# Optimization experiments

Hardware: AMD Instinct MI355X
Metric: run time of the kernel (lower is better)

The kernel has to match this reference:

```python
import jax, jax.numpy as jnp
import numpy as np

NEG_SLOPE = 0.2  # PyG GATConv default negative_slope
N_GRAPHS = 128


def gat_conv(x, src, dst, w, a_src, a_dst, b):
    """PyG GATConv (v1), concat=True. x:[N,F], src/dst:[E] (self-loops included),
    w:[F,H*C], a_src/a_dst:[H,C], b:[H*C]."""
    N = x.shape[0]
    H, C = a_src.shape
    h = (x @ w).reshape(N, H, C)                      # [N,H,C]
    e = (h * a_src).sum(-1)[src] + (h * a_dst).sum(-1)[dst]  # [E,H]
    e = jnp.where(e > 0, e, NEG_SLOPE * e)            # leaky_relu
    m = jax.ops.segment_max(e, dst, num_segments=N)   # per-dst softmax max
    ex = jnp.exp(e - m[dst])
    s = jax.ops.segment_sum(ex, dst, num_segments=N)
    alpha = ex / (s[dst] + 1e-16)                     # [E,H]
    out = jax.ops.segment_sum(h[src] * alpha[:, :, None], dst, num_segments=N)
    return out.reshape(N, H * C) + b


def pool(x, batch, num_graphs):
    """concat(global_mean_pool, global_max_pool)."""
    ones = jnp.ones((x.shape[0],), x.dtype)
    cnt = jax.ops.segment_sum(ones, batch, num_segments=num_graphs)
    mean = jax.ops.segment_sum(x, batch, num_segments=num_graphs) / jnp.maximum(cnt, 1.0)[:, None]
    mx = jax.ops.segment_max(x, batch, num_segments=num_graphs)
    return jnp.concatenate([mean, mx], axis=-1)


def setup_inputs() -> dict:
    key = jax.random.key(0)
    ks = jax.random.split(key, 30)
    N, E, G = 100000, 800000, N_GRAPHS
    F_in, H, C = 260, 4, 64
    HC = H * C  # 256

    def lin(k, i, o):
        return (jax.random.normal(k, (i, o), jnp.float32) * (1.0 / np.sqrt(i)))

    def att(k):
        return jax.random.normal(k, (H, C), jnp.float32) * 0.1

    return {
        "x": jax.random.normal(ks[0], (N, F_in), jnp.float32),
        "edge_index": jax.random.randint(ks[1], (2, E), 0, N),
        "batch": jnp.sort(jax.random.randint(ks[2], (N,), 0, G)),
        "gat1_w": lin(ks[3], F_in, HC), "gat1_as": att(ks[4]), "gat1_ad": att(ks[5]),
        "gat1_b": jnp.zeros((HC,), jnp.float32),
        "lin1_w": lin(ks[6], HC, C), "lin1_b": jnp.zeros((C,), jnp.float32),
        "gat2_w": lin(ks[7], C, HC), "gat2_as": att(ks[8]), "gat2_ad": att(ks[9]),
        "gat2_b": jnp.zeros((HC,), jnp.float32),
        "lin2_w": lin(ks[10], HC, C), "lin2_b": jnp.zeros((C,), jnp.float32),
        "sum_w": lin(ks[11], 4 * C, 2 * C), "sum_b": jnp.zeros((2 * C,), jnp.float32),
        "sh1_w": lin(ks[12], 2 * C, C), "sh1_b": jnp.zeros((C,), jnp.float32),
        "sh2_w": lin(ks[13], C, C), "sh2_b": jnp.zeros((C,), jnp.float32),
        "sh3_w": lin(ks[14], C, C), "sh3_b": jnp.zeros((C,), jnp.float32),
        "reg_w": lin(ks[15], C, 32), "reg_b": jnp.zeros((32,), jnp.float32),
    }


def reference(x, edge_index, batch,
              gat1_w, gat1_as, gat1_ad, gat1_b, lin1_w, lin1_b,
              gat2_w, gat2_as, gat2_ad, gat2_b, lin2_w, lin2_b,
              sum_w, sum_b, sh1_w, sh1_b, sh2_w, sh2_b, sh3_w, sh3_b,
              reg_w, reg_b):
    N = x.shape[0]
    loop = jnp.arange(N)
    src = jnp.concatenate([edge_index[0], loop])  # add_self_loops=True
    dst = jnp.concatenate([edge_index[1], loop])

    h = gat_conv(x, src, dst, gat1_w, gat1_as, gat1_ad, gat1_b)
    h = jax.nn.selu(h @ lin1_w + lin1_b)
    x1 = pool(h, batch, N_GRAPHS)                 # [G, 2C]

    h = gat_conv(h, src, dst, gat2_w, gat2_as, gat2_ad, gat2_b)
    h = jax.nn.selu(h @ lin2_w + lin2_b)
    x2 = pool(h, batch, N_GRAPHS)                 # [G, 2C]

    z = jnp.concatenate([x1, x2], axis=-1) @ sum_w + sum_b
    z = jax.nn.selu(z @ sh1_w + sh1_b)
    z = jax.nn.selu(z @ sh2_w + sh2_b)
    z = jax.nn.selu(z @ sh3_w + sh3_b)
    return z @ reg_w + reg_b                      # [G, 32]
```

## Files before the change

### kernel.cpp

```cpp
#include <hip/hip_runtime.h>
#include <hip/hip_bf16.h>
#include <cstdint>

#define NEG_SLOPE 0.2f
#define HEADS 4
#define CH 64
#define HC 256
#define F_IN 260
#define KPAD1 288
#define NGRAPH 128

typedef __attribute__((ext_vector_type(8))) short bf16x8;
typedef __attribute__((ext_vector_type(8))) unsigned short u16x8;
typedef __attribute__((ext_vector_type(4))) float f32x4;

__device__ __forceinline__ float seluf(float x){
    const float sc=1.0507009873554805f, al=1.6732632423543772f;
    return x>0.f ? sc*x : sc*al*(__expf(x)-1.f);
}
__device__ __forceinline__ unsigned fenc(float x){
    unsigned u=__float_as_uint(x);
    return (u&0x80000000u)? ~u : (u|0x80000000u);
}
__device__ __forceinline__ float fdec(unsigned e){
    unsigned u = (e&0x80000000u)? (e&0x7fffffffu) : ~e;
    return __uint_as_float(u);
}
__device__ __forceinline__ float bf2f(unsigned short u){
    return __uint_as_float(((unsigned)u)<<16);
}
__device__ __forceinline__ unsigned short f2bf_raw(float x){
    unsigned u = __float_as_uint(x);
    unsigned rounded = u + 0x7fffu + ((u >> 16) & 1u);
    return (unsigned short)(rounded >> 16);
}
__device__ __forceinline__ void gload_lds16(const void* g, void* l){
    __builtin_amdgcn_global_load_lds(
        (const __attribute__((address_space(1))) void*)g,
        (__attribute__((address_space(3))) void*)l, 16, 0, 0);
}

__global__ void fill_u32_kernel(unsigned* p, unsigned v, int n){
    int i = blockIdx.x*blockDim.x + threadIdx.x;
    for (; i<n; i += gridDim.x*blockDim.x) p[i]=v;
}

__global__ void degree_kernel(const int* __restrict__ ei, int* __restrict__ deg, int E){
    int i = blockIdx.x*blockDim.x+threadIdx.x;
    for (; i<E; i+=gridDim.x*blockDim.x) atomicAdd(&deg[ei[E+i]], 1);
}

__global__ void scan_ph1(const int* __restrict__ deg, int* __restrict__ bsum, int N){
    __shared__ int sd[256];
    int base = blockIdx.x*1024;
    int t = threadIdx.x;
    int tot=0;
    for(int u=0;u<4;u++){ int i = base + t*4+u; tot += (i<N)? deg[i]:0; }
    sd[t]=tot; __syncthreads();
    for(int off=128; off; off>>=1){ if(t<off) sd[t]+=sd[t+off]; __syncthreads(); }
    if(t==0) bsum[blockIdx.x]=sd[0];
}
__global__ void scan_ph2(int* bsum, int nb, int* rowptr, int N, int E){
    if(threadIdx.x==0 && blockIdx.x==0){
        int run=0;
        for(int b=0;b<nb;b++){ int v=bsum[b]; bsum[b]=run; run+=v; }
        rowptr[N]=E;
    }
}
__global__ void scan_ph3(const int* __restrict__ deg, const int* __restrict__ bsum,
                         int* __restrict__ rowptr, int N){
    __shared__ int sd[256];
    int base = blockIdx.x*1024;
    int t = threadIdx.x;
    int v[4]; int tot=0;
    for(int u=0;u<4;u++){ int i=base+t*4+u; v[u] = (i<N)? deg[i]:0; tot+=v[u]; }
    sd[t]=tot; __syncthreads();
    for(int off=1; off<256; off<<=1){
        int add = (t>=off)? sd[t-off] : 0;
        __syncthreads();
        sd[t] += add;
        __syncthreads();
    }
    int pre = bsum[blockIdx.x] + ((t==0)?0: sd[t-1]);
    for(int u=0;u<4;u++){ int i=base+t*4+u; if(i<N){ rowptr[i]=pre; pre+=v[u]; } }
}

__global__ void scatter_kernel(const int* __restrict__ ei, const int* __restrict__ rowptr,
                               int* __restrict__ fil, int* __restrict__ col, int E){
    int i = blockIdx.x*blockDim.x+threadIdx.x;
    for(; i<E; i+=gridDim.x*blockDim.x){
        int s = ei[i], d = ei[E+i];
        int p = atomicAdd(&fil[d],1);
        col[rowptr[d]+p] = s;
    }
}

__global__ void cvt_x_kernel(const float* __restrict__ x, unsigned* __restrict__ xb, int N){
    int i = blockIdx.x*blockDim.x+threadIdx.x;
    int total = N*36;
    for (; i<total; i+=gridDim.x*blockDim.x){
        int row = i/36;
        int c = (i - row*36)*8;
        const float* src = x + (size_t)row*F_IN + c;
        float v[8];
        if (c + 8 <= F_IN){
            float4 a = *(const float4*)src;
            float4 b = *(const float4*)(src+4);
            v[0]=a.x; v[1]=a.y; v[2]=a.z; v[3]=a.w;
            v[4]=b.x; v[5]=b.y; v[6]=b.z; v[7]=b.w;
        } else {
            #pragma unroll
            for (int k=0;k<8;k++) v[k] = (c+k < F_IN) ? src[k] : 0.f;
        }
        unsigned d[4];
        #pragma unroll
        for (int k=0;k<4;k++)
            d[k] = (unsigned)f2bf_raw(v[2*k]) | ((unsigned)f2bf_raw(v[2*k+1])<<16);
        *(int4*)(xb + (size_t)row*144 + (c>>1)) = make_int4((int)d[0],(int)d[1],(int)d[2],(int)d[3]);
    }
}

__global__ void cvt_wT_kernel(const float* __restrict__ w, __hip_bfloat16* __restrict__ wt,
                              int K, int NC, int Kpad){
    int i = blockIdx.x*blockDim.x+threadIdx.x;
    if (i >= NC*Kpad) return;
    int n = i / Kpad, k = i - n*Kpad;
    wt[i] = __float2bfloat16(k < K ? w[(size_t)k*NC + n] : 0.f);
}

template<int BN, int FS>
__global__ __launch_bounds__(512, 4) void mfma_gemm_kernel(
    const __hip_bfloat16* __restrict__ A, int Kpad,
    const __hip_bfloat16* __restrict__ Bt,
    const float* __restrict__ bias, int act,
    __hip_bfloat16* __restrict__ Cb,
    const float* __restrict__ asrc, const float* __restrict__ adst,
    float* __restrict__ ss, float* __restrict__ sdv,
    int M, int NC)
{
    constexpr int NF = BN/32;
    constexpr int WN = BN/2;
    constexpr int TP = WN + 8;
    __shared__ __align__(16) char lds[32768];

    int tid  = threadIdx.x;
    int lane = tid & 63;
    int w    = tid >> 6;
    int wr = w >> 1, wc = w & 1;
    int row0 = blockIdx.x * 128;
    int col0 = blockIdx.y * BN;
    int fr   = lane & 15;
    int koff = (lane >> 4) * 16;

    f32x4 acc[2][NF];
    #pragma unroll
    for (int i=0;i<2;i++)
        #pragma unroll
        for (int j=0;j<NF;j++) acc[i][j] = (f32x4){0.f,0.f,0.f,0.f};

    int lrow = lane >> 2;
    int lcolB = (lane & 3) * 16;
    int ktiles = Kpad >> 5;

    auto stage = [&](int kt, int pb){
        int k0b = kt*64;
        char* Asb = lds + pb*8192;
        char* Bsb = lds + 16384 + pb*(BN*64);
        {
            int gr = row0 + w*16 + lrow; if (gr > M-1) gr = M-1;
            gload_lds16((const char*)A + (size_t)gr*Kpad*2 + k0b + lcolB,
                        Asb + w*1024 + lrow*64 + lcolB);
        }
        if (w < BN/16){
            int gn = col0 + w*16 + lrow;
            gload_lds16((const char*)Bt + (size_t)gn*Kpad*2 + k0b + lcolB,
                        Bsb + w*1024 + lrow*64 + lcolB);
        }
    };

    stage(0, 0);
    __syncthreads();
    for (int kt=0; kt<ktiles; kt++){
        int pb = kt & 1;
        if (kt+1 < ktiles) stage(kt+1, pb^1);
        const char* Ab = lds + pb*8192;
        const char* Bb = lds + 16384 + pb*(BN*64);
        bf16x8 a[2], b[NF];
        a[0] = *(const bf16x8*)(Ab + (wr*32 +      fr)*64 + koff);
        a[1] = *(const bf16x8*)(Ab + (wr*32 + 16 + fr)*64 + koff);
        #pragma unroll
        for (int nt=0; nt<NF; nt++)
            b[nt] = *(const bf16x8*)(Bb + (wc*WN + nt*16 + fr)*64 + koff);
        #pragma unroll
        for (int mt=0; mt<2; mt++)
            #pragma unroll
            for (int nt=0; nt<NF; nt++)
                acc[mt][nt] = __builtin_amdgcn_mfma_f32_16x16x32_bf16(a[mt], b[nt], acc[mt][nt], 0, 0, 0);
        __syncthreads();
    }

    if (FS){
        float asv[NF], adv[NF];
        #pragma unroll
        for (int nt=0; nt<NF; nt++){
            int gc = col0 + wc*WN + nt*16 + fr;
            asv[nt] = asrc[gc];
            adv[nt] = adst[gc];
        }
        int head = (col0 + wc*WN) >> 6;
        #pragma unroll
        for (int mt=0; mt<2; mt++){
            #pragma unroll
            for (int r=0; r<4; r++){
                float ts=0.f, td=0.f;
                #pragma unroll
                for (int nt=0; nt<NF; nt++){
                    ts = fmaf(acc[mt][nt][r], asv[nt], ts);
                    td = fmaf(acc[mt][nt][r], adv[nt], td);
                }
                #pragma unroll
                for (int off=1; off<16; off<<=1){
                    ts += __shfl_xor(ts, off);
                    td += __shfl_xor(td, off);
                }
                if (fr==0){
                    int gr = row0 + wr*32 + mt*16 + (lane>>4)*4 + r;
                    if (gr < M){ ss[gr*4+head]=ts; sdv[gr*4+head]=td; }
                }
            }
        }
    }

    char* ct = lds + w*(16*TP*2);
    int c0 = col0 + wc*WN;
    #pragma unroll
    for (int mt=0; mt<2; mt++){
        #pragma unroll
        for (int nt=0; nt<NF; nt++){
            #pragma unroll
            for (int r=0; r<4; r++){
                float v = acc[mt][nt][r];
                if (bias) v += bias[c0 + nt*16 + fr];
                if (act)  v = seluf(v);
                int tr = (lane>>4)*4 + r;
                *(unsigned short*)(ct + tr*(TP*2) + (nt*16+fr)*2) = f2bf_raw(v);
            }
        }
        constexpr int CPR = WN/8;
        constexpr int RPP = 64/CPR;
        #pragma unroll
        for (int p=0; p<16/RPP; p++){
            int tr = p*RPP + lane/CPR;
            int ch = lane % CPR;
            int4 v = *(const int4*)(ct + tr*(TP*2) + ch*16);
            int gr = row0 + wr*32 + mt*16 + tr;
            if (gr < M)
                *(int4*)((char*)Cb + ((size_t)gr*NC + c0 + ch*8)*2) = v;
        }
    }
}

__global__ void aggregate_fused_kernel(const __hip_bfloat16* __restrict__ h,
                                       const float* __restrict__ ss, const float* __restrict__ sdv,
                                       const int* __restrict__ rowptr, const int* __restrict__ col,
                                       const float* __restrict__ bias,
                                       __hip_bfloat16* __restrict__ outp, int N){
    int node = blockIdx.x*4 + (threadIdx.x>>6);
    if (node >= N) return;
    int lane = threadIdx.x & 63;
    int s = lane >> 4;
    int t = lane & 15;
    int hh = t >> 2;
    const unsigned short* hp = (const unsigned short*)h;

    float ad = sdv[node*4+hh];
    float e0 = ss[node*4+hh] + ad;
    e0 = e0>0.f ? e0 : NEG_SLOPE*e0;

    int jb = rowptr[node], je = rowptr[node+1];

    float m = (s==0) ? e0 : -1e30f;
    for (int j0 = jb; j0 < je; j0 += 8){
        int jA = j0 + s, jB = j0 + s + 4;
        if (jA < je){
            float e = ss[col[jA]*4+hh] + ad;
            m = fmaxf(m, e>0.f ? e : NEG_SLOPE*e);
        }
        if (jB < je){
            float e = ss[col[jB]*4+hh] + ad;
            m = fmaxf(m, e>0.f ? e : NEG_SLOPE*e);
        }
    }
    m = fmaxf(m, __shfl_xor(m, 16));
    m = fmaxf(m, __shfl_xor(m, 32));

    float acc[16];
    float psum;
    {
        float sa = (s==0) ? __expf(e0-m) : 0.f;
        psum = sa;
        const unsigned short* base = hp + (size_t)node*HC + t*16;
        u16x8 v0 = *(const u16x8*)(base);
        u16x8 v1 = *(const u16x8*)(base + 8);
        #pragma unroll
        for (int k=0;k<8;k++){
            acc[k]   = sa * bf2f(v0[k]);
            acc[8+k] = sa * bf2f(v1[k]);
        }
    }
    for (int j0 = jb; j0 < je; j0 += 8){
        int jA = j0 + s;
        int jB = j0 + s + 4;
        int scA = (jA < je) ? col[jA] : node;
        int scB = (jB < je) ? col[jB] : node;
        const unsigned short* bA = hp + (size_t)scA*HC + t*16;
        const unsigned short* bB = hp + (size_t)scB*HC + t*16;
        u16x8 a0 = *(const u16x8*)bA;
        u16x8 a1 = *(const u16x8*)(bA + 8);
        u16x8 b0 = *(const u16x8*)bB;
        u16x8 b1 = *(const u16x8*)(bB + 8);
        float eA = ss[scA*4+hh] + ad;
        float eB = ss[scB*4+hh] + ad;
        eA = eA>0.f ? eA : NEG_SLOPE*eA;
        eB = eB>0.f ? eB : NEG_SLOPE*eB;
        float pA = (jA < je) ? __expf(eA - m) : 0.f;
        float pB = (jB < je) ? __expf(eB - m) : 0.f;
        psum += pA + pB;
        #pragma unroll
        for (int k=0;k<8;k++){
            acc[k]   = fmaf(pA, bf2f(a0[k]), acc[k]);
            acc[8+k] = fmaf(pA, bf2f(a1[k]), acc[8+k]);
        }
        #pragma unroll
        for (int k=0;k<8;k++){
            acc[k]   = fmaf(pB, bf2f(b0[k]), acc[k]);
            acc[8+k] = fmaf(pB, bf2f(b1[k]), acc[8+k]);
        }
    }

    #pragma unroll
    for (int k=0;k<16;k++){
        acc[k] += __shfl_xor(acc[k], 16);
        acc[k] += __shfl_xor(acc[k], 32);
    }
    psum += __shfl_xor(psum, 16);
    psum += __shfl_xor(psum, 32);

    if (s==0){
        float inv = 1.f / psum;
        unsigned d[8];
        #pragma unroll
        for (int k=0;k<8;k++){
            unsigned lo = f2bf_raw(fmaf(acc[2*k],   inv, bias[t*16 + 2*k]));
            unsigned hi = f2bf_raw(fmaf(acc[2*k+1], inv, bias[t*16 + 2*k+1]));
            d[k] = lo | (hi<<16);
        }
        unsigned short* op = (unsigned short*)outp + (size_t)node*HC + t*16;
        int4 w0 = make_int4((int)d[0], (int)d[1], (int)d[2], (int)d[3]);
        int4 w1 = make_int4((int)d[4], (int)d[5], (int)d[6], (int)d[7]);
        *(int4*)op = w0;
        *(int4*)(op + 8) = w1;
    }
}

template<int DO_COUNT>
__global__ void pool_kernel(const __hip_bfloat16* __restrict__ hs, const int* __restrict__ batch,
                            float* __restrict__ psum, unsigned* __restrict__ pmax,
                            int* __restrict__ cnt, int N){
    int c = threadIdx.x & 63;
    int sub = threadIdx.x >> 6;
    int n0 = blockIdx.x*128 + sub*32;
    const unsigned short* hp = (const unsigned short*)hs;
    float s = 0.f, mx = -__builtin_inff();
    int cur = -1, rl = 0;
    for (int j=0; j<32; j++){
        int n = n0 + j;
        if (n >= N) break;
        int g = batch[n];
        if (g != cur){
            if (cur >= 0){
                atomicAdd(&psum[cur*64+c], s);
                atomicMax(&pmax[cur*64+c], fenc(mx));
                if (DO_COUNT && c==0) atomicAdd(&cnt[cur], rl);
            }
            cur = g; s = 0.f; mx = -__builtin_inff(); rl = 0;
        }
        float v = bf2f(hp[(size_t)n*64 + c]);
        s += v; mx = fmaxf(mx, v); rl++;
    }
    if (cur >= 0){
        atomicAdd(&psum[cur*64+c], s);
        atomicMax(&pmax[cur*64+c], fenc(mx));
        if (DO_COUNT && c==0) atomicAdd(&cnt[cur], rl);
    }
}

__global__ void pool_final_kernel(const float* __restrict__ psum, const unsigned* __restrict__ pmax,
                                  const int* __restrict__ cnt, float* __restrict__ x, int G){
    int i = blockIdx.x*blockDim.x+threadIdx.x;
    if (i >= G*64) return;
    int g=i>>6, c=i&63;
    float cf = fmaxf((float)cnt[g], 1.f);
    x[g*128 + c] = psum[i]/cf;
    x[g*128 + 64 + c] = fdec(pmax[i]);
}

__global__ __launch_bounds__(128) void head_kernel(
    const float* __restrict__ x1, const float* __restrict__ x2,
    const float* __restrict__ sw, const float* __restrict__ sb,
    const float* __restrict__ w1, const float* __restrict__ b1,
    const float* __restrict__ w2, const float* __restrict__ b2,
    const float* __restrict__ w3, const float* __restrict__ b3,
    const float* __restrict__ rw, const float* __restrict__ rb,
    float* __restrict__ out)
{
    int g = blockIdx.x, t = threadIdx.x;
    __shared__ float v[256], z1[128], z2[64], z3[64], z4[64];
    v[t] = x1[g*128+t];
    v[128+t] = x2[g*128+t];
    __syncthreads();
    float a = sb[t];
    for(int k=0;k<256;k++) a = fmaf(v[k], sw[k*128+t], a);
    z1[t] = a;
    __syncthreads();
    if(t<64){
        float a2 = b1[t];
        for(int k=0;k<128;k++) a2 = fmaf(z1[k], w1[k*64+t], a2);
        z2[t] = seluf(a2);
    }
    __syncthreads();
    if(t<64){
        float a3 = b2[t];
        for(int k=0;k<64;k++) a3 = fmaf(z2[k], w2[k*64+t], a3);
        z3[t] = seluf(a3);
    }
    __syncthreads();
    if(t<64){
        float a4 = b3[t];
        for(int k=0;k<64;k++) a4 = fmaf(z3[k], w3[k*64+t], a4);
        z4[t] = seluf(a4);
    }
    __syncthreads();
    if(t<32){
        float a5 = rb[t];
        for(int k=0;k<64;k++) a5 = fmaf(z4[k], rw[k*32+t], a5);
        out[g*32+t] = a5;
    }
}

extern "C" void kernel_launch(void* const* d_in, const int* in_sizes, int n_in,
                              void* d_out, int out_size, void* d_ws, size_t ws_size,
                              hipStream_t stream)
{
    const float* x    = (const float*)d_in[0];
    const int*   ei   = (const int*)d_in[1];
    const int*   batch= (const int*)d_in[2];
    const float* g1w  = (const float*)d_in[3];
    const float* g1as = (const float*)d_in[4];
    const float* g1ad = (const float*)d_in[5];
    const float* g1b  = (const float*)d_in[6];
    const float* l1w  = (const float*)d_in[7];
    const float* l1b  = (const float*)d_in[8];
    const float* g2w  = (const float*)d_in[9];
    const float* g2as = (const float*)d_in[10];
    const float* g2ad = (const float*)d_in[11];
    const float* g2b  = (const float*)d_in[12];
    const float* l2w  = (const float*)d_in[13];
    const float* l2b  = (const float*)d_in[14];
    const float* sw   = (const float*)d_in[15];
    const float* sb   = (const float*)d_in[16];
    const float* s1w  = (const float*)d_in[17];
    const float* s1b  = (const float*)d_in[18];
    const float* s2w  = (const float*)d_in[19];
    const float* s2b  = (const float*)d_in[20];
    const float* s3w  = (const float*)d_in[21];
    const float* s3b  = (const float*)d_in[22];
    const float* rw   = (const float*)d_in[23];
    const float* rb   = (const float*)d_in[24];
    float* out = (float*)d_out;

    const int N = in_sizes[0] / F_IN;
    const int E = in_sizes[1] / 2;
    const int G = NGRAPH;

    char* ws = (char*)d_ws;
    size_t off = 0;
    auto alloc = [&](size_t bytes)->void*{
        void* p = ws + off;
        off += (bytes + 255) & ~(size_t)255;
        return p;
    };
    int* deg     = (int*)alloc((size_t)2*N*4);
    int* fil     = deg + N;
    int* rowptr  = (int*)alloc(((size_t)N+1)*4);
    int* col     = (int*)alloc((size_t)E*4);
    int* bsum    = (int*)alloc(1024);
    int* zpool   = (int*)alloc((size_t)(128 + 2*G*64)*4);
    int*   cnt = zpool;
    float* PS1 = (float*)(zpool + 128);
    float* PS2 = PS1 + G*64;
    unsigned* PM1 = (unsigned*)alloc((size_t)2*G*64*4);
    unsigned* PM2 = PM1 + G*64;
    float* X1    = (float*)alloc((size_t)G*128*4);
    float* X2    = (float*)alloc((size_t)G*128*4);
    __hip_bfloat16* Xb  = (__hip_bfloat16*)alloc((size_t)N*KPAD1*2);
    __hip_bfloat16* W1t = (__hip_bfloat16*)alloc((size_t)HC*KPAD1*2);
    __hip_bfloat16* L1t = (__hip_bfloat16*)alloc((size_t)CH*HC*2);
    __hip_bfloat16* W2t = (__hip_bfloat16*)alloc((size_t)HC*CH*2);
    __hip_bfloat16* L2t = (__hip_bfloat16*)alloc((size_t)CH*HC*2);
    __hip_bfloat16* Abf = (__hip_bfloat16*)alloc((size_t)N*HC*2);
    __hip_bfloat16* Bbf = (__hip_bfloat16*)alloc((size_t)N*HC*2);
    __hip_bfloat16* HSb = (__hip_bfloat16*)alloc((size_t)N*CH*2);
    float* SCS   = (float*)alloc((size_t)N*HEADS*4);
    float* SCD   = (float*)alloc((size_t)N*HEADS*4);
    (void)ws_size; (void)n_in; (void)out_size;

    const unsigned ENC_NEG_INF = 0x007FFFFFu;
    int nb = (N+1023)/1024;

    fill_u32_kernel<<<256,256,0,stream>>>((unsigned*)deg, 0u, 2*N);
    fill_u32_kernel<<<64,256,0,stream>>>((unsigned*)zpool, 0u, 128 + 2*G*64);
    fill_u32_kernel<<<64,256,0,stream>>>(PM1, ENC_NEG_INF, 2*G*64);

    degree_kernel<<<1024,256,0,stream>>>(ei, deg, E);
    scan_ph1<<<nb,256,0,stream>>>(deg, bsum, N);
    scan_ph2<<<1,64,0,stream>>>(bsum, nb, rowptr, N, E);
    scan_ph3<<<nb,256,0,stream>>>(deg, bsum, rowptr, N);
    scatter_kernel<<<1024,256,0,stream>>>(ei, rowptr, fil, col, E);

    cvt_x_kernel<<<2048,256,0,stream>>>(x, (unsigned*)Xb, N);
    cvt_wT_kernel<<<(HC*KPAD1+255)/256,256,0,stream>>>(g1w, W1t, F_IN, HC, KPAD1);
    cvt_wT_kernel<<<(CH*HC+255)/256,256,0,stream>>>(l1w, L1t, HC, CH, HC);
    cvt_wT_kernel<<<(HC*CH+255)/256,256,0,stream>>>(g2w, W2t, CH, HC, CH);
    cvt_wT_kernel<<<(CH*HC+255)/256,256,0,stream>>>(l2w, L2t, HC, CH, HC);

    int nodeBlocks = (N+3)/4;
    dim3 gA((N+127)/128, 2);
    dim3 gL((N+127)/128, 1);

    mfma_gemm_kernel<128,1><<<gA,512,0,stream>>>(Xb, KPAD1, W1t, nullptr, 0, Abf,
                                                 g1as, g1ad, SCS, SCD, N, HC);
    aggregate_fused_kernel<<<nodeBlocks,256,0,stream>>>(Abf, SCS, SCD, rowptr, col, g1b, Bbf, N);
    mfma_gemm_kernel<64,0><<<gL,512,0,stream>>>(Bbf, HC, L1t, l1b, 1, HSb,
                                                nullptr, nullptr, nullptr, nullptr, N, CH);
    pool_kernel<1><<<(N+127)/128,256,0,stream>>>(HSb, batch, PS1, PM1, cnt, N);
    pool_final_kernel<<<(G*64+255)/256,256,0,stream>>>(PS1, PM1, cnt, X1, G);

    mfma_gemm_kernel<128,1><<<gA,512,0,stream>>>(HSb, CH, W2t, nullptr, 0, Abf,
                                                 g2as, g2ad, SCS, SCD, N, HC);
    aggregate_fused_kernel<<<nodeBlocks,256,0,stream>>>(Abf, SCS, SCD, rowptr, col, g2b, Bbf, N);
    mfma_gemm_kernel<64,0><<<gL,512,0,stream>>>(Bbf, HC, L2t, l2b, 1, HSb,
                                                nullptr, nullptr, nullptr, nullptr, N, CH);
    pool_kernel<0><<<(N+127)/128,256,0,stream>>>(HSb, batch, PS2, PM2, nullptr, N);
    pool_final_kernel<<<(G*64+255)/256,256,0,stream>>>(PS2, PM2, cnt, X2, G);

    head_kernel<<<G,128,0,stream>>>(X1, X2, sw, sb, s1w, s1b, s2w, s2b, s3w, s3b, rw, rb, out);
}
```

Before: 482.7 us.

## Fuse global mean/max pooling into the lin GEMM epilogue and drop pool kernels

The linear GEMM that follows each GAT layer now applies bias and SELU, stages the bf16 tile in LDS, and computes per-graph sum, max and count with atomics directly from that tile. The separate pool kernels are removed, and the second layer skips writing its activations to global memory entirely. This removes two launches and an extra read of the hidden features, plus one write. The cost is extra LDS per GEMM block, which may lower occupancy. Leaky-ReLU in the aggregation kernel is also rewritten as a branch-free fmaxf.

```diff
diff --git a/kernel.cpp b/kernel.cpp
--- a/kernel.cpp
+++ b/kernel.cpp
@@ -128,7 +128,7 @@
     wt[i] = __float2bfloat16(k < K ? w[(size_t)k*NC + n] : 0.f);
 }
 
-template<int BN, int FS>
+template<int BN, int FS, int POOL, int STORE>
 __global__ __launch_bounds__(512, 4) void mfma_gemm_kernel(
     const __hip_bfloat16* __restrict__ A, int Kpad,
     const __hip_bfloat16* __restrict__ Bt,
@@ -136,12 +136,16 @@
     __hip_bfloat16* __restrict__ Cb,
     const float* __restrict__ asrc, const float* __restrict__ adst,
     float* __restrict__ ss, float* __restrict__ sdv,
+    const int* __restrict__ batch, float* __restrict__ psum,
+    unsigned* __restrict__ pmax, int* __restrict__ cnt,
     int M, int NC)
 {
     constexpr int NF = BN/32;
     constexpr int WN = BN/2;
     constexpr int TP = WN + 8;
-    __shared__ __align__(16) char lds[32768];
+    constexpr int STAGE = 16384 + 2*BN*64;
+    constexpr int LDSB  = POOL ? (STAGE + 128*72*2) : 32768;
+    __shared__ __align__(16) char lds[LDSB];
 
     int tid  = threadIdx.x;
     int lane = tid & 63;
@@ -197,6 +201,60 @@
             for (int nt=0; nt<NF; nt++)
                 acc[mt][nt] = __builtin_amdgcn_mfma_f32_16x16x32_bf16(a[mt], b[nt], acc[mt][nt], 0, 0, 0);
         __syncthreads();
+    }
+
+    if (POOL){
+        unsigned short* tile = (unsigned short*)(lds + STAGE);
+        #pragma unroll
+        for (int mt=0; mt<2; mt++)
+            #pragma unroll
+            for (int nt=0; nt<NF; nt++)
+                #pragma unroll
+                for (int r=0; r<4; r++){
+                    float v = acc[mt][nt][r] + bias[wc*WN + nt*16 + fr];
+                    v = seluf(v);
+                    int tr = wr*32 + mt*16 + (lane>>4)*4 + r;
+                    tile[tr*72 + wc*WN + nt*16 + fr] = f2bf_raw(v);
+                }
+        __syncthreads();
+        if (STORE){
+            #pragma unroll
+            for (int p=0; p<2; p++){
+                int idx = tid + p*512;
+                int r = idx >> 3, ch = idx & 7;
+                int gr = row0 + r;
+                if (gr < M)
+                    *(int4*)((char*)Cb + ((size_t)gr*NC + ch*8)*2) =
+                        *(const int4*)((const char*)tile + r*144 + ch*16);
+            }
+        }
+        int c  = tid & 63;
+        int g8 = tid >> 6;
+        float sum = 0.f, mx = -__builtin_inff();
+        int cur = -1, rl = 0;
+        #pragma unroll 1
+        for (int j=0; j<16; j++){
+            int r = g8*16 + j;
+            int n = row0 + r;
+            if (n >= M) break;
+            int g = batch[n];
+            if (g != cur){
+                if (cur >= 0){
+                    atomicAdd(&psum[cur*64+c], sum);
+                    atomicMax(&pmax[cur*64+c], fenc(mx));
+                    if (POOL==1 && c==0) atomicAdd(&cnt[cur], rl);
+                }
+                cur = g; sum = 0.f; mx = -__builtin_inff(); rl = 0;
+            }
+            float v = bf2f(tile[r*72 + c]);
+            sum += v; mx = fmaxf(mx, v); rl++;
+        }
+        if (cur >= 0){
+            atomicAdd(&psum[cur*64+c], sum);
+            atomicMax(&pmax[cur*64+c], fenc(mx));
+            if (POOL==1 && c==0) atomicAdd(&cnt[cur], rl);
+        }
+        return;
     }
 
     if (FS){
@@ -275,7 +333,7 @@
 
     float ad = sdv[node*4+hh];
     float e0 = ss[node*4+hh] + ad;
-    e0 = e0>0.f ? e0 : NEG_SLOPE*e0;
+    e0 = fmaxf(e0, NEG_SLOPE*e0);
 
     int jb = rowptr[node], je = rowptr[node+1];
 
@@ -284,11 +342,11 @@
         int jA = j0 + s, jB = j0 + s + 4;
         if (jA < je){
             float e = ss[col[jA]*4+hh] + ad;
-            m = fmaxf(m, e>0.f ? e : NEG_SLOPE*e);
+            m = fmaxf(m, fmaxf(e, NEG_SLOPE*e));
         }
         if (jB < je){
             float e = ss[col[jB]*4+hh] + ad;
-            m = fmaxf(m, e>0.f ? e : NEG_SLOPE*e);
+            m = fmaxf(m, fmaxf(e, NEG_SLOPE*e));
         }
     }
     m = fmaxf(m, __shfl_xor(m, 16));
@@ -321,8 +379,8 @@
         u16x8 b1 = *(const u16x8*)(bB + 8);
         float eA = ss[scA*4+hh] + ad;
         float eB = ss[scB*4+hh] + ad;
-        eA = eA>0.f ? eA : NEG_SLOPE*eA;
-        eB = eB>0.f ? eB : NEG_SLOPE*eB;
+        eA = fmaxf(eA, NEG_SLOPE*eA);
+        eB = fmaxf(eB, NEG_SLOPE*eB);
         float pA = (jA < je) ? __expf(eA - m) : 0.f;
         float pB = (jB < je) ? __expf(eB - m) : 0.f;
         psum += pA + pB;
@@ -360,38 +418,6 @@
         int4 w1 = make_int4((int)d[4], (int)d[5], (int)d[6], (int)d[7]);
         *(int4*)op = w0;
         *(int4*)(op + 8) = w1;
-    }
-}
-
-template<int DO_COUNT>
-__global__ void pool_kernel(const __hip_bfloat16* __restrict__ hs, const int* __restrict__ batch,
-                            float* __restrict__ psum, unsigned* __restrict__ pmax,
-                            int* __restrict__ cnt, int N){
-    int c = threadIdx.x & 63;
-    int sub = threadIdx.x >> 6;
-    int n0 = blockIdx.x*128 + sub*32;
-    const unsigned short* hp = (const unsigned short*)hs;
-    float s = 0.f, mx = -__builtin_inff();
-    int cur = -1, rl = 0;
-    for (int j=0; j<32; j++){
-        int n = n0 + j;
-        if (n >= N) break;
-        int g = batch[n];
-        if (g != cur){
-            if (cur >= 0){
-                atomicAdd(&psum[cur*64+c], s);
-                atomicMax(&pmax[cur*64+c], fenc(mx));
-                if (DO_COUNT && c==0) atomicAdd(&cnt[cur], rl);
-            }
-            cur = g; s = 0.f; mx = -__builtin_inff(); rl = 0;
-        }
-        float v = bf2f(hp[(size_t)n*64 + c]);
-        s += v; mx = fmaxf(mx, v); rl++;
-    }
-    if (cur >= 0){
-        atomicAdd(&psum[cur*64+c], s);
-        atomicMax(&pmax[cur*64+c], fenc(mx));
-        if (DO_COUNT && c==0) atomicAdd(&cnt[cur], rl);
     }
 }
 
@@ -538,20 +564,22 @@
     dim3 gA((N+127)/128, 2);
     dim3 gL((N+127)/128, 1);
 
-    mfma_gemm_kernel<128,1><<<gA,512,0,stream>>>(Xb, KPAD1, W1t, nullptr, 0, Abf,
-                                                 g1as, g1ad, SCS, SCD, N, HC);
+    mfma_gemm_kernel<128,1,0,1><<<gA,512,0,stream>>>(Xb, KPAD1, W1t, nullptr, 0, Abf,
+                                                     g1as, g1ad, SCS, SCD,
+                                                     nullptr, nullptr, nullptr, nullptr, N, HC);
     aggregate_fused_kernel<<<nodeBlocks,256,0,stream>>>(Abf, SCS, SCD, rowptr, col, g1b, Bbf, N);
-    mfma_gemm_kernel<64,0><<<gL,512,0,stream>>>(Bbf, HC, L1t, l1b, 1, HSb,
-                                                nullptr, nullptr, nullptr, nullptr, N, CH);
-    pool_kernel<1><<<(N+127)/128,256,0,stream>>>(HSb, batch, PS1, PM1, cnt, N);
+    mfma_gemm_kernel<64,0,1,1><<<gL,512,0,stream>>>(Bbf, HC, L1t, l1b, 1, HSb,
+                                                    nullptr, nullptr, nullptr, nullptr,
+                                                    batch, PS1, PM1, cnt, N, CH);
     pool_final_kernel<<<(G*64+255)/256,256,0,stream>>>(PS1, PM1, cnt, X1, G);
 
-    mfma_gemm_kernel<128,1><<<gA,512,0,stream>>>(HSb, CH, W2t, nullptr, 0, Abf,
-                                                 g2as, g2ad, SCS, SCD, N, HC);
+    mfma_gemm_kernel<128,1,0,1><<<gA,512,0,stream>>>(HSb, CH, W2t, nullptr, 0, Abf,
+                                                     g2as, g2ad, SCS, SCD,
+                                                     nullptr, nullptr, nullptr, nullptr, N, HC);
     aggregate_fused_kernel<<<nodeBlocks,256,0,stream>>>(Abf, SCS, SCD, rowptr, col, g2b, Bbf, N);
-    mfma_gemm_kernel<64,0><<<gL,512,0,stream>>>(Bbf, HC, L2t, l2b, 1, HSb,
-                                                nullptr, nullptr, nullptr, nullptr, N, CH);
-    pool_kernel<0><<<(N+127)/128,256,0,stream>>>(HSb, batch, PS2, PM2, nullptr, N);
+    mfma_gemm_kernel<64,0,2,0><<<gL,512,0,stream>>>(Bbf, HC, L2t, l2b, 1, nullptr,
+                                                    nullptr, nullptr, nullptr, nullptr,
+                                                    batch, PS2, PM2, nullptr, N, CH);
     pool_final_kernel<<<(G*64+255)/256,256,0,stream>>>(PS2, PM2, cnt, X2, G);
 
     head_kernel<<<G,128,0,stream>>>(X1, X2, sw, sb, s1w, s1b, s2w, s2b, s3w, s3b, rw, rb, out);
```

New measurement: 462.7 us. 4.1% less time.
